# Performance work log

Hardware: AMD Instinct MI355X
Metric: run time of the kernel (lower is better)

## Reference

```python
import jax, jax.numpy as jnp
import numpy as np

B, C, H, W = 4, 64, 64, 64
NUM_HEADS = 4
INTER = 64
OUT_PLANE = 64
TOP_K = 5
BN_EPS = 1e-5


def setup_inputs() -> dict:
    key = jax.random.key(0)
    ks = jax.random.split(key, 24)
    d = {}
    d['x'] = jax.random.normal(ks[0], (B, C, H, W), dtype=jnp.float32)
    oc = INTER * NUM_HEADS
    s_in = 1.0 / np.sqrt(C)
    s_oc = 1.0 / np.sqrt(oc)
    s_op = 1.0 / np.sqrt(OUT_PLANE)
    d['wk'] = jax.random.normal(ks[1], (oc, C), dtype=jnp.float32) * s_in
    d['bk'] = jax.random.normal(ks[2], (oc,), dtype=jnp.float32) * s_in
    d['wq'] = jax.random.normal(ks[3], (oc, C), dtype=jnp.float32) * s_in
    d['bq'] = jax.random.normal(ks[4], (oc,), dtype=jnp.float32) * s_in
    d['wv'] = jax.random.normal(ks[5], (oc, C), dtype=jnp.float32) * s_in
    d['bv'] = jax.random.normal(ks[6], (oc,), dtype=jnp.float32) * s_in
    d['wp'] = jax.random.normal(ks[7], (OUT_PLANE, oc), dtype=jnp.float32) * s_oc
    d['bp'] = jax.random.normal(ks[8], (OUT_PLANE,), dtype=jnp.float32) * s_oc
    d['w1'] = jax.random.normal(ks[9], (OUT_PLANE, OUT_PLANE), dtype=jnp.float32) * s_op
    d['b1'] = jax.random.normal(ks[10], (OUT_PLANE,), dtype=jnp.float32) * s_op
    d['w2'] = jax.random.normal(ks[11], (OUT_PLANE, OUT_PLANE), dtype=jnp.float32) * s_op
    d['b2'] = jax.random.normal(ks[12], (OUT_PLANE,), dtype=jnp.float32) * s_op
    d['g1'] = 1.0 + 0.1 * jax.random.normal(ks[13], (OUT_PLANE,), dtype=jnp.float32)
    d['beta1'] = 0.1 * jax.random.normal(ks[14], (OUT_PLANE,), dtype=jnp.float32)
    d['m1'] = 0.1 * jax.random.normal(ks[15], (OUT_PLANE,), dtype=jnp.float32)
    d['v1'] = 1.0 + 0.1 * jax.random.uniform(ks[16], (OUT_PLANE,), dtype=jnp.float32)
    d['g2'] = 1.0 + 0.1 * jax.random.normal(ks[17], (OUT_PLANE,), dtype=jnp.float32)
    d['beta2'] = 0.1 * jax.random.normal(ks[18], (OUT_PLANE,), dtype=jnp.float32)
    d['m2'] = 0.1 * jax.random.normal(ks[19], (OUT_PLANE,), dtype=jnp.float32)
    d['v2'] = 1.0 + 0.1 * jax.random.uniform(ks[20], (OUT_PLANE,), dtype=jnp.float32)
    return d


def _conv1x1(x, w, b):
    return jnp.einsum('bchw,oc->bohw', x, w) + b[None, :, None, None]


def _l2norm(x, axis):
    n = jnp.sqrt(jnp.sum(x * x, axis=axis, keepdims=True))
    return x / jnp.maximum(n, 1e-12)


def _bn(x, g, be, m, v):
    scale = g / jnp.sqrt(v + BN_EPS)
    return (x - m[None, :, None, None]) * scale[None, :, None, None] + be[None, :, None, None]


def _laplacian(topk_idx, feats):
    # topk_idx: (b, N, K) int32; feats: (b, heads, N, F)
    b, heads, N, Fd = feats.shape
    K = topk_idx.shape[-1]
    src = jnp.repeat(jnp.arange(N), K)  # (N*K,)

    def one(idx, f):  # idx (N,K), f (heads,N,F)
        dst = idx.reshape(-1)  # (N*K,)
        # A = topk edges + self-loops; row degrees (dim=1 sum)
        deg = jnp.zeros((N,), feats.dtype).at[src].add(1.0) + 1.0
        norm = jnp.maximum(deg ** -0.5, 1e-9)
        w = norm[src] * norm[dst]  # (N*K,)
        gathered = f[:, dst, :] * w[None, :, None]  # (heads, N*K, F)
        agg = jax.vmap(lambda g_: jnp.zeros((N, Fd), feats.dtype).at[src].add(g_))(gathered)
        # self-loop contribution (value 1, norm[i]^2)
        return agg + (norm * norm)[None, :, None] * f

    return jax.vmap(one)(topk_idx, feats)


def reference(x, wk, bk, wq, bq, wv, bv, wp, bp, w1, b1, w2, b2,
              g1, beta1, m1, v1, g2, beta2, m2, v2):
    b, c, h, w = x.shape
    N = h * w
    # q/k/v: (b, heads, N, inter)
    k = _conv1x1(x, wk, bk).reshape(b, NUM_HEADS, INTER, N).transpose(0, 1, 3, 2)
    q = _conv1x1(x, wq, bq).reshape(b, NUM_HEADS, INTER, N).transpose(0, 1, 3, 2)
    v = _conv1x1(x, wv, bv).reshape(b, NUM_HEADS, INTER, N).transpose(0, 1, 3, 2)
    k = _l2norm(k, -1)
    q = _l2norm(q, -1)
    # hypergraph: cosine similarity over channels, top-k neighbors per node
    x_flat = x.reshape(b, c, N)
    xn = _l2norm(x_flat, 1)
    sim = jnp.einsum('bcn,bcm->bnm', xn, xn)  # (b, N, N)
    _, idx = jax.lax.top_k(sim, TOP_K)  # (b, N, K)
    k = _laplacian(idx, k)
    v = _laplacian(idx, v)
    # hydra attention: kv summed over nodes, broadcast back over q
    kv = jnp.einsum('bhnf,bhnf->bhf', k, v)[:, :, None, :]  # (b, heads, 1, inter)
    hy = q * kv  # (b, heads, N, inter)
    hy = hy.transpose(0, 1, 3, 2).reshape(b, NUM_HEADS * INTER, h, w)
    out = _conv1x1(hy, wp, bp)
    out = jax.nn.relu(_bn(_conv1x1(out, w1, b1), g1, beta1, m1, v1))
    out = jax.nn.relu(_bn(_conv1x1(out, w2, b2), g2, beta2, m2, v2))
    return out
```

## Files before the change

kernel.cpp:

```cpp
#include <hip/hip_runtime.h>
#include <math.h>

#define NB 4
#define NC 64
#define NN 4096
#define NH 4

typedef __attribute__((ext_vector_type(8))) short bf16x8;
typedef __attribute__((ext_vector_type(4))) float f32x4;

__device__ __forceinline__ unsigned int bf16rne(float v) {
    unsigned int u = __float_as_uint(v);
    return (u + 0x7fffu + ((u >> 16) & 1u)) >> 16;
}

__device__ __forceinline__ void ins5k(unsigned int (&tk)[5], unsigned int key) {
    unsigned int n0 = max(tk[0], key);
    unsigned int n1 = min(tk[0], max(tk[1], key));
    unsigned int n2 = min(tk[1], max(tk[2], key));
    unsigned int n3 = min(tk[2], max(tk[3], key));
    unsigned int n4 = min(tk[3], max(tk[4], key));
    tk[0]=n0; tk[1]=n1; tk[2]=n2; tk[3]=n3; tk[4]=n4;
}

__device__ __forceinline__ void split8(const float* v, uint4& hw4, uint4& lw4) {
    unsigned int hw[4], lw[4];
    #pragma unroll
    for (int p = 0; p < 4; ++p) {
        float v0 = v[p*2], v1 = v[p*2+1];
        unsigned int h0 = bf16rne(v0), h1 = bf16rne(v1);
        float r0 = v0 - __uint_as_float(h0 << 16);
        float r1 = v1 - __uint_as_float(h1 << 16);
        unsigned int l0 = bf16rne(r0), l1 = bf16rne(r1);
        hw[p] = h0 | (h1 << 16);
        lw[p] = l0 | (l1 << 16);
    }
    hw4 = make_uint4(hw[0], hw[1], hw[2], hw[3]);
    lw4 = make_uint4(lw[0], lw[1], lw[2], lw[3]);
}

__global__ __launch_bounds__(256) void k_pre(
    const float* __restrict__ x,
    const float* __restrict__ wk, const float* __restrict__ wq, const float* __restrict__ wv,
    unsigned short* __restrict__ hl, float* __restrict__ nrm,
    unsigned short* __restrict__ wsb)
{
    __shared__ float redn[4][64];
    int blk = blockIdx.x;
    int t = threadIdx.x;
    if (blk >= 256) {
        int r = (blk - 256)*256 + t;
        int mat = r >> 8, oc = r & 255;
        const float* wsrc = (mat==0) ? wk : ((mat==1) ? wq : wv);
        float wrow[64];
        #pragma unroll
        for (int g = 0; g < 16; ++g)
            *(float4*)&wrow[g*4] = *(const float4*)(wsrc + (size_t)oc*64 + g*4);
        unsigned short* wo = wsb + (size_t)r*128;
        #pragma unroll
        for (int g = 0; g < 8; ++g) {
            uint4 hw4, lw4;
            split8(&wrow[g*8], hw4, lw4);
            *(uint4*)(wo + g*8)      = hw4;
            *(uint4*)(wo + 64 + g*8) = lw4;
        }
        return;
    }
    int lane = t & 63, g = t >> 6;
    int node = blk*64 + lane;
    const float* xb = x + ((size_t)(node >> 12))*NC*NN + (node & (NN-1));
    float vals[16];
    float ss = 0.f;
    #pragma unroll
    for (int i = 0; i < 16; ++i) {
        vals[i] = xb[(size_t)(g*16 + i)*NN];
        ss += vals[i]*vals[i];
    }
    redn[g][lane] = ss;
    __syncthreads();
    float st = redn[0][lane] + redn[1][lane] + redn[2][lane] + redn[3][lane];
    float rn = 1.f / fmaxf(sqrtf(st), 1e-12f);
    if (g == 0) nrm[node] = sqrtf(st);
    float nv[16];
    #pragma unroll
    for (int i = 0; i < 16; ++i) nv[i] = vals[i] * rn;
    unsigned short* ho = hl + (size_t)node*128 + g*16;
    #pragma unroll
    for (int gg = 0; gg < 2; ++gg) {
        uint4 hw4, lw4;
        split8(&nv[gg*8], hw4, lw4);
        *(uint4*)(ho + gg*8)      = hw4;
        *(uint4*)(ho + 64 + gg*8) = lw4;
    }
}

__global__ __launch_bounds__(256, 2) void k_qkv(
    const unsigned short* __restrict__ hl, const float* __restrict__ nrm,
    const unsigned short* __restrict__ wsb,
    const float* __restrict__ bk, const float* __restrict__ bq, const float* __restrict__ bv,
    float* __restrict__ qo, float* __restrict__ ko, float* __restrict__ vo)
{
    int blk = blockIdx.x;
    int nt  = blk & 63;
    int rem = blk >> 6;
    int mat = rem % 3, b = rem / 3;
    const float* bias = (mat==0) ? bk : ((mat==1) ? bq : bv);
    float* outp       = (mat==0) ? ko : ((mat==1) ? qo : vo);
    int t = threadIdx.x, lane = t & 63, h = t >> 6;
    int ln = lane & 15, kh = lane >> 4;

    bf16x8 ah0[4], ah1[4], al0[4], al1[4];
    const unsigned short* wb2 = wsb + ((size_t)(mat*256 + h*64 + ln))*128 + kh*8;
    #pragma unroll
    for (int s = 0; s < 4; ++s) {
        const unsigned short* p = wb2 + (size_t)s*16*128;
        ah0[s] = *(const bf16x8*)(p);
        ah1[s] = *(const bf16x8*)(p + 32);
        al0[s] = *(const bf16x8*)(p + 64);
        al1[s] = *(const bf16x8*)(p + 96);
    }
    float4 bj[4];
    #pragma unroll
    for (int s = 0; s < 4; ++s) bj[s] = *(const float4*)(bias + h*64 + s*16 + kh*4);

    int n0base = nt*64;
    const unsigned short* xb2 = hl + ((size_t)b*NN + n0base + ln)*128 + kh*8;
    #pragma unroll
    for (int j = 0; j < 4; ++j) {
        const unsigned short* p = xb2 + (size_t)j*16*128;
        bf16x8 bh0 = *(const bf16x8*)(p);
        bf16x8 bh1 = *(const bf16x8*)(p + 32);
        bf16x8 bl0 = *(const bf16x8*)(p + 64);
        bf16x8 bl1 = *(const bf16x8*)(p + 96);
        int n = n0base + j*16 + ln;
        float sc = nrm[(size_t)b*NN + n];
        f32x4 av[4];
        #pragma unroll
        for (int s = 0; s < 4; ++s) {
            f32x4 acc = {0.f, 0.f, 0.f, 0.f};
            acc = __builtin_amdgcn_mfma_f32_16x16x32_bf16(ah0[s], bh0, acc, 0,0,0);
            acc = __builtin_amdgcn_mfma_f32_16x16x32_bf16(ah1[s], bh1, acc, 0,0,0);
            acc = __builtin_amdgcn_mfma_f32_16x16x32_bf16(al0[s], bh0, acc, 0,0,0);
            acc = __builtin_amdgcn_mfma_f32_16x16x32_bf16(al1[s], bh1, acc, 0,0,0);
            acc = __builtin_amdgcn_mfma_f32_16x16x32_bf16(ah0[s], bl0, acc, 0,0,0);
            acc = __builtin_amdgcn_mfma_f32_16x16x32_bf16(ah1[s], bl1, acc, 0,0,0);
            av[s][0] = acc[0]*sc + bj[s].x;
            av[s][1] = acc[1]*sc + bj[s].y;
            av[s][2] = acc[2]*sc + bj[s].z;
            av[s][3] = acc[3]*sc + bj[s].w;
        }
        float* ob = outp + (((size_t)(b*NH + h))*NN + n)*64 + kh*4;
        if (mat != 2) {
            float ss = 0.f;
            #pragma unroll
            for (int s = 0; s < 4; ++s)
                ss += av[s][0]*av[s][0] + av[s][1]*av[s][1]
                    + av[s][2]*av[s][2] + av[s][3]*av[s][3];
            ss += __shfl_xor(ss, 16);
            ss += __shfl_xor(ss, 32);
            float rn = 1.f / fmaxf(sqrtf(ss), 1e-12f);
            #pragma unroll
            for (int s = 0; s < 4; ++s)
                *(float4*)(ob + s*16) = make_float4(av[s][0]*rn, av[s][1]*rn,
                                                    av[s][2]*rn, av[s][3]*rn);
        } else {
            #pragma unroll
            for (int s = 0; s < 4; ++s)
                *(float4*)(ob + s*16) = make_float4(av[s][0], av[s][1],
                                                    av[s][2], av[s][3]);
        }
    }
}

__device__ __forceinline__ void ctile(const bf16x8& ah0, const bf16x8& ah1,
                                      const bf16x8& al0, const bf16x8& al1,
                                      const bf16x8& bh0, const bf16x8& bh1,
                                      const bf16x8& bl0, const bf16x8& bl1,
                                      unsigned int (&tk)[4][5], unsigned int inv)
{
    f32x4 accP = {2.0f, 2.0f, 2.0f, 2.0f};
    f32x4 accQ = {0.f, 0.f, 0.f, 0.f};
    f32x4 accR = {0.f, 0.f, 0.f, 0.f};
    accP = __builtin_amdgcn_mfma_f32_16x16x32_bf16(ah0, bh0, accP, 0,0,0);
    accQ = __builtin_amdgcn_mfma_f32_16x16x32_bf16(al0, bh0, accQ, 0,0,0);
    accR = __builtin_amdgcn_mfma_f32_16x16x32_bf16(ah0, bl0, accR, 0,0,0);
    accP = __builtin_amdgcn_mfma_f32_16x16x32_bf16(ah1, bh1, accP, 0,0,0);
    accQ = __builtin_amdgcn_mfma_f32_16x16x32_bf16(al1, bh1, accQ, 0,0,0);
    accR = __builtin_amdgcn_mfma_f32_16x16x32_bf16(ah1, bl1, accR, 0,0,0);
    #pragma unroll
    for (int r = 0; r < 4; ++r) {
        float v = (accP[r] + accQ[r]) + accR[r];
        unsigned int key = (__float_as_uint(v) & 0xFFFFF000u) | inv;
        ins5k(tk[r], key);
    }
}

__global__ __launch_bounds__(256, 2)
void k_topk(const unsigned short* __restrict__ hl, unsigned int* __restrict__ pk)
{
    int blk = blockIdx.x;
    int cs = blk & 7;
    int rg = (blk >> 3) & 15;
    int b  = blk >> 7;
    int t = threadIdx.x, lane = t & 63, wave = t >> 6;
    int ln = lane & 15, kh = lane >> 4;
    const unsigned short* hb = hl + (size_t)b*NN*128;

    const unsigned short* ap0 = hb + (size_t)(rg*256 + wave*64 + ln)*128 + kh*8;
    bf16x8 a0h0 = *(const bf16x8*)(ap0);
    bf16x8 a0h1 = *(const bf16x8*)(ap0 + 32);
    bf16x8 a0l0 = *(const bf16x8*)(ap0 + 64);
    bf16x8 a0l1 = *(const bf16x8*)(ap0 + 96);
    const unsigned short* ap1 = ap0 + 16*128;
    bf16x8 a1h0 = *(const bf16x8*)(ap1);
    bf16x8 a1h1 = *(const bf16x8*)(ap1 + 32);
    bf16x8 a1l0 = *(const bf16x8*)(ap1 + 64);
    bf16x8 a1l1 = *(const bf16x8*)(ap1 + 96);
    const unsigned short* ap2 = ap0 + 32*128;
    bf16x8 a2h0 = *(const bf16x8*)(ap2);
    bf16x8 a2h1 = *(const bf16x8*)(ap2 + 32);
    bf16x8 a2l0 = *(const bf16x8*)(ap2 + 64);
    bf16x8 a2l1 = *(const bf16x8*)(ap2 + 96);
    const unsigned short* ap3 = ap0 + 48*128;
    bf16x8 a3h0 = *(const bf16x8*)(ap3);
    bf16x8 a3h1 = *(const bf16x8*)(ap3 + 32);
    bf16x8 a3l0 = *(const bf16x8*)(ap3 + 64);
    bf16x8 a3l1 = *(const bf16x8*)(ap3 + 96);

    unsigned int tk0[4][5], tk1[4][5], tk2[4][5], tk3[4][5];
    #pragma unroll
    for (int r=0;r<4;++r)
        #pragma unroll
        for (int kk=0;kk<5;++kk) { tk0[r][kk]=0u; tk1[r][kk]=0u; tk2[r][kk]=0u; tk3[r][kk]=0u; }

    int colbase = cs*512;
    unsigned int inv0 = 4095u - (unsigned int)(colbase + ln);

    const unsigned short* bp = hb + (size_t)(colbase + ln)*128 + kh*8;
    bf16x8 Ah0 = *(const bf16x8*)(bp);
    bf16x8 Ah1 = *(const bf16x8*)(bp + 32);
    bf16x8 Al0 = *(const bf16x8*)(bp + 64);
    bf16x8 Al1 = *(const bf16x8*)(bp + 96);
    bf16x8 Bh0, Bh1, Bl0, Bl1;

    for (int t5 = 0; t5 < 32; t5 += 2) {
        {
            const unsigned short* p = bp + (size_t)(t5+1)*16*128;
            Bh0 = *(const bf16x8*)(p);
            Bh1 = *(const bf16x8*)(p + 32);
            Bl0 = *(const bf16x8*)(p + 64);
            Bl1 = *(const bf16x8*)(p + 96);
        }
        {
            unsigned int inv = inv0 - (unsigned int)(t5*16);
            ctile(a0h0,a0h1,a0l0,a0l1, Ah0,Ah1,Al0,Al1, tk0, inv);
            ctile(a1h0,a1h1,a1l0,a1l1, Ah0,Ah1,Al0,Al1, tk1, inv);
            ctile(a2h0,a2h1,a2l0,a2l1, Ah0,Ah1,Al0,Al1, tk2, inv);
            ctile(a3h0,a3h1,a3l0,a3l1, Ah0,Ah1,Al0,Al1, tk3, inv);
        }
        {
            int m = (t5+2 < 32) ? (t5+2) : 0;
            const unsigned short* p = bp + (size_t)m*16*128;
            Ah0 = *(const bf16x8*)(p);
            Ah1 = *(const bf16x8*)(p + 32);
            Al0 = *(const bf16x8*)(p + 64);
            Al1 = *(const bf16x8*)(p + 96);
        }
        {
            unsigned int inv = inv0 - (unsigned int)((t5+1)*16);
            ctile(a0h0,a0h1,a0l0,a0l1, Bh0,Bh1,Bl0,Bl1, tk0, inv);
            ctile(a1h0,a1h1,a1l0,a1l1, Bh0,Bh1,Bl0,Bl1, tk1, inv);
            ctile(a2h0,a2h1,a2l0,a2l1, Bh0,Bh1,Bl0,Bl1, tk2, inv);
            ctile(a3h0,a3h1,a3l0,a3l1, Bh0,Bh1,Bl0,Bl1, tk3, inv);
        }
    }

    #pragma unroll
    for (int m = 1; m < 16; m <<= 1) {
        #pragma unroll
        for (int r=0;r<4;++r) {
            unsigned int o0[5], o1[5], o2[5], o3[5];
            #pragma unroll
            for (int kk=0;kk<5;++kk) {
                o0[kk] = (unsigned int)__shfl_xor((int)tk0[r][kk], m);
                o1[kk] = (unsigned int)__shfl_xor((int)tk1[r][kk], m);
                o2[kk] = (unsigned int)__shfl_xor((int)tk2[r][kk], m);
                o3[kk] = (unsigned int)__shfl_xor((int)tk3[r][kk], m);
            }
            #pragma unroll
            for (int kk=0;kk<5;++kk) {
                ins5k(tk0[r], o0[kk]); ins5k(tk1[r], o1[kk]);
                ins5k(tk2[r], o2[kk]); ins5k(tk3[r], o3[kk]);
            }
        }
    }
    if (ln == 0) {
        int rowb = rg*256 + wave*64 + kh*4;
        #pragma unroll
        for (int r=0;r<4;++r) {
            size_t b0 = (((size_t)b*NN + rowb + r)*8 + cs)*5;
            size_t b1 = (((size_t)b*NN + rowb + 16 + r)*8 + cs)*5;
            size_t b2 = (((size_t)b*NN + rowb + 32 + r)*8 + cs)*5;
            size_t b3 = (((size_t)b*NN + rowb + 48 + r)*8 + cs)*5;
            #pragma unroll
            for (int kk=0;kk<5;++kk) {
                pk[b0+kk] = tk0[r][kk]; pk[b1+kk] = tk1[r][kk];
                pk[b2+kk] = tk2[r][kk]; pk[b3+kk] = tk3[r][kk];
            }
        }
    }
}

__global__ __launch_bounds__(256) void k_kv(const float* __restrict__ ko, const float* __restrict__ vo,
                                            const unsigned int* __restrict__ pk, float* __restrict__ part)
{
    int blk = blockIdx.x;
    int chunk = blk & 31, bh = blk >> 5, b = bh >> 2;
    int t = threadIdx.x;
    __shared__ int idxl[128][5];
    __shared__ float red[4][64];
    if (t < 128) {
        int n = chunk*128 + t;
        const uint4* pp = (const uint4*)(pk + ((size_t)b*NN + n)*40);
        unsigned int bk5[5] = {0u,0u,0u,0u,0u};
        #pragma unroll
        for (int e = 0; e < 10; ++e) {
            uint4 v4 = pp[e];
            ins5k(bk5, v4.x); ins5k(bk5, v4.y); ins5k(bk5, v4.z); ins5k(bk5, v4.w);
        }
        #pragma unroll
        for (int kk=0;kk<5;++kk) idxl[t][kk] = 4095 - (int)(bk5[kk] & 0xFFFu);
    }
    __syncthreads();
    int f = t & 63, g = t >> 6;
    const float* kb = ko + (size_t)bh*NN*64;
    const float* vb = vo + (size_t)bh*NN*64;
    float acc = 0.f;
    for (int i2 = 0; i2 < 32; ++i2) {
        int nl = g*32 + i2;
        int n = chunk*128 + nl;
        const int* ip = idxl[nl];
        int j0 = ip[0], j1 = ip[1], j2 = ip[2], j3 = ip[3], j4 = ip[4];
        float lk = kb[(size_t)n*64+f] + kb[(size_t)j0*64+f] + kb[(size_t)j1*64+f]
                 + kb[(size_t)j2*64+f] + kb[(size_t)j3*64+f] + kb[(size_t)j4*64+f];
        float lv = vb[(size_t)n*64+f] + vb[(size_t)j0*64+f] + vb[(size_t)j1*64+f]
                 + vb[(size_t)j2*64+f] + vb[(size_t)j3*64+f] + vb[(size_t)j4*64+f];
        acc += lk*lv;
    }
    red[g][f] = acc;
    __syncthreads();
    if (t < 64) {
        float s2 = red[0][t] + red[1][t] + red[2][t] + red[3][t];
        part[((size_t)bh*64 + t)*32 + chunk] = s2;
    }
}

__global__ __launch_bounds__(256) void k_out(
    const float* __restrict__ qo, const float* __restrict__ wp, const float* __restrict__ part,
    const float* __restrict__ bp,
    const float* __restrict__ w1, const float* __restrict__ b1,
    const float* __restrict__ w2, const float* __restrict__ b2,
    const float* __restrict__ g1, const float* __restrict__ be1,
    const float* __restrict__ m1, const float* __restrict__ v1,
    const float* __restrict__ g2, const float* __restrict__ be2,
    const float* __restrict__ m2, const float* __restrict__ v2,
    float* __restrict__ outp)
{
    int b  = blockIdx.x >> 6;
    int n0 = (blockIdx.x & 63)*64;
    __shared__ __align__(16) float qs[256*68];
    __shared__ __align__(16) float ws2[256*68];
    __shared__ __align__(16) float t0[64*68];
    int t = threadIdx.x;
    {
        int f = t & 63, sub = t >> 6;
        #pragma unroll
        for (int h = 0; h < 4; ++h) {
            const float* qb = qo + (((size_t)(b*4+h))*NN + n0)*64 + f;
            for (int nl = sub; nl < 64; nl += 4)
                qs[(h*64+f)*68 + nl] = qb[(size_t)nl*64];
        }
    }
    {
        const float* pp = part + ((size_t)b*256 + t)*32;
        float s = 0.f;
        #pragma unroll
        for (int c2 = 0; c2 < 32; ++c2) s += pp[c2];
        float kvv = s * (1.f/36.f);
        for (int o = 0; o < 64; ++o)
            ws2[t*68 + o] = wp[(size_t)o*256 + t] * kvv;
    }
    __syncthreads();
    int tr = t >> 4, tc = t & 15;
    float acc[4][4];
    #pragma unroll
    for (int i=0;i<4;++i) {
        float bb = bp[tr*4+i];
        #pragma unroll
        for (int j=0;j<4;++j) acc[i][j] = bb;
    }
    #pragma unroll 8
    for (int hf = 0; hf < 256; ++hf) {
        float4 a4 = *(const float4*)&ws2[hf*68 + tr*4];
        float4 b4 = *(const float4*)&qs[hf*68 + tc*4];
        float av[4]={a4.x,a4.y,a4.z,a4.w}, bvv[4]={b4.x,b4.y,b4.z,b4.w};
        #pragma unroll
        for (int i=0;i<4;++i)
            #pragma unroll
            for (int j=0;j<4;++j)
                acc[i][j] += av[i]*bvv[j];
    }
    #pragma unroll
    for (int i=0;i<4;++i)
        *(float4*)&t0[(tr*4+i)*68 + tc*4] = make_float4(acc[i][0],acc[i][1],acc[i][2],acc[i][3]);
    __syncthreads();
    #pragma unroll
    for (int s = 0; s < 16; ++s) {
        int e = t + 256*s;
        ws2[(e & 63)*68 + (e >> 6)] = w1[e];
    }
    __syncthreads();
    float acc2[4][4];
    #pragma unroll
    for (int i=0;i<4;++i)
        #pragma unroll
        for (int j=0;j<4;++j) acc2[i][j] = 0.f;
    #pragma unroll 8
    for (int c = 0; c < 64; ++c) {
        float4 a4 = *(const float4*)&ws2[c*68 + tr*4];
        float4 b4 = *(const float4*)&t0[c*68 + tc*4];
        float av[4]={a4.x,a4.y,a4.z,a4.w}, bvv[4]={b4.x,b4.y,b4.z,b4.w};
        #pragma unroll
        for (int i=0;i<4;++i)
            #pragma unroll
            for (int j=0;j<4;++j)
                acc2[i][j] += av[i]*bvv[j];
    }
    #pragma unroll
    for (int i=0;i<4;++i) {
        int o = tr*4+i;
        float sc = g1[o] / sqrtf(v1[o] + 1e-5f);
        float bb = b1[o], mm = m1[o], bt = be1[o];
        float4 r;
        r.x = fmaxf((acc2[i][0]+bb-mm)*sc + bt, 0.f);
        r.y = fmaxf((acc2[i][1]+bb-mm)*sc + bt, 0.f);
        r.z = fmaxf((acc2[i][2]+bb-mm)*sc + bt, 0.f);
        r.w = fmaxf((acc2[i][3]+bb-mm)*sc + bt, 0.f);
        *(float4*)&qs[o*68 + tc*4] = r;
    }
    __syncthreads();
    #pragma unroll
    for (int s = 0; s < 16; ++s) {
        int e = t + 256*s;
        ws2[(e & 63)*68 + (e >> 6)] = w2[e];
    }
    __syncthreads();
    float acc3[4][4];
    #pragma unroll
    for (int i=0;i<4;++i)
        #pragma unroll
        for (int j=0;j<4;++j) acc3[i][j] = 0.f;
    #pragma unroll 8
    for (int c = 0; c < 64; ++c) {
        float4 a4 = *(const float4*)&ws2[c*68 + tr*4];
        float4 b4 = *(const float4*)&qs[c*68 + tc*4];
        float av[4]={a4.x,a4.y,a4.z,a4.w}, bvv[4]={b4.x,b4.y,b4.z,b4.w};
        #pragma unroll
        for (int i=0;i<4;++i)
            #pragma unroll
            for (int j=0;j<4;++j)
                acc3[i][j] += av[i]*bvv[j];
    }
    #pragma unroll
    for (int i=0;i<4;++i) {
        int o = tr*4+i;
        float sc = g2[o] / sqrtf(v2[o] + 1e-5f);
        float bb = b2[o], mm = m2[o], bt = be2[o];
        float4 r;
        r.x = fmaxf((acc3[i][0]+bb-mm)*sc + bt, 0.f);
        r.y = fmaxf((acc3[i][1]+bb-mm)*sc + bt, 0.f);
        r.z = fmaxf((acc3[i][2]+bb-mm)*sc + bt, 0.f);
        r.w = fmaxf((acc3[i][3]+bb-mm)*sc + bt, 0.f);
        *(float4*)&t0[o*68 + tc*4] = r;
    }
    __syncthreads();
    float* ob = outp + ((size_t)b*64)*NN + n0;
    #pragma unroll
    for (int s = 0; s < 16; ++s) {
        int e = t + 256*s;
        int o = e >> 6, nl = e & 63;
        ob[(size_t)o*NN + nl] = t0[o*68 + nl];
    }
}

extern "C" void kernel_launch(void* const* d_in, const int* in_sizes, int n_in,
                              void* d_out, int out_size, void* d_ws, size_t ws_size,
                              hipStream_t stream)
{
    (void)in_sizes; (void)n_in; (void)out_size; (void)ws_size;
    const float* x  = (const float*)d_in[0];
    const float* wk = (const float*)d_in[1];
    const float* bk = (const float*)d_in[2];
    const float* wq = (const float*)d_in[3];
    const float* bq = (const float*)d_in[4];
    const float* wv = (const float*)d_in[5];
    const float* bv = (const float*)d_in[6];
    const float* wp = (const float*)d_in[7];
    const float* bp = (const float*)d_in[8];
    const float* w1 = (const float*)d_in[9];
    const float* b1 = (const float*)d_in[10];
    const float* w2 = (const float*)d_in[11];
    const float* b2 = (const float*)d_in[12];
    const float* g1 = (const float*)d_in[13];
    const float* be1= (const float*)d_in[14];
    const float* m1 = (const float*)d_in[15];
    const float* v1 = (const float*)d_in[16];
    const float* g2 = (const float*)d_in[17];
    const float* be2= (const float*)d_in[18];
    const float* m2 = (const float*)d_in[19];
    const float* v2 = (const float*)d_in[20];
    float* out = (float*)d_out;

    float* ws = (float*)d_ws;
    unsigned short* hlb = (unsigned short*)ws;  ws += (size_t)NB*NN*128/2;
    unsigned short* wsb = (unsigned short*)ws;  ws += (size_t)768*128/2;
    float* nrm  = ws;  ws += (size_t)NB*NN;
    float* qbuf = ws;  ws += (size_t)NB*NH*NN*64;
    float* kbuf = ws;  ws += (size_t)NB*NH*NN*64;
    float* vbuf = ws;  ws += (size_t)NB*NH*NN*64;
    float* part = ws;  ws += (size_t)16*64*32;
    unsigned int* pk = (unsigned int*)ws;  ws += (size_t)NB*NN*40;

    k_pre<<<259, 256, 0, stream>>>(x, wk, wq, wv, hlb, nrm, wsb);
    k_qkv<<<768, 256, 0, stream>>>(hlb, nrm, wsb, bk, bq, bv, qbuf, kbuf, vbuf);
    k_topk<<<512, 256, 0, stream>>>(hlb, pk);
    k_kv<<<512, 256, 0, stream>>>(kbuf, vbuf, pk, part);
    k_out<<<256, 256, 0, stream>>>(qbuf, wp, part, bp, w1,b1, w2,b2,
                                   g1,be1,m1,v1, g2,be2,m2,v2, out);
}
```

Measured before the change: 144.4 us.

## Halve k_out tile width to double blocks and shrink shared memory

The output kernel now processes 32 nodes per block instead of 64, launching 512 blocks with much smaller shared-memory buffers. It no longer builds a kv-scaled copy of the projection weights in LDS; instead it reads wp rows directly from global memory and scales them on the fly with kv kept in LDS. The top-k similarity tile also merges the third split-precision MFMA accumulator into the first, saving registers and one add. The aim is higher occupancy and less LDS setup. In exchange each block issues more global weight loads and the per-thread tiles are smaller.

```diff
diff --git a/kernel.cpp b/kernel.cpp
--- a/kernel.cpp
+++ b/kernel.cpp
@@ -180,16 +180,15 @@
 {
     f32x4 accP = {2.0f, 2.0f, 2.0f, 2.0f};
     f32x4 accQ = {0.f, 0.f, 0.f, 0.f};
-    f32x4 accR = {0.f, 0.f, 0.f, 0.f};
     accP = __builtin_amdgcn_mfma_f32_16x16x32_bf16(ah0, bh0, accP, 0,0,0);
     accQ = __builtin_amdgcn_mfma_f32_16x16x32_bf16(al0, bh0, accQ, 0,0,0);
-    accR = __builtin_amdgcn_mfma_f32_16x16x32_bf16(ah0, bl0, accR, 0,0,0);
     accP = __builtin_amdgcn_mfma_f32_16x16x32_bf16(ah1, bh1, accP, 0,0,0);
     accQ = __builtin_amdgcn_mfma_f32_16x16x32_bf16(al1, bh1, accQ, 0,0,0);
-    accR = __builtin_amdgcn_mfma_f32_16x16x32_bf16(ah1, bl1, accR, 0,0,0);
+    accP = __builtin_amdgcn_mfma_f32_16x16x32_bf16(ah0, bl0, accP, 0,0,0);
+    accP = __builtin_amdgcn_mfma_f32_16x16x32_bf16(ah1, bl1, accP, 0,0,0);
     #pragma unroll
     for (int r = 0; r < 4; ++r) {
-        float v = (accP[r] + accQ[r]) + accR[r];
+        float v = accP[r] + accQ[r];
         unsigned int key = (__float_as_uint(v) & 0xFFFFF000u) | inv;
         ins5k(tk[r], key);
     }
@@ -366,19 +365,20 @@
     const float* __restrict__ m2, const float* __restrict__ v2,
     float* __restrict__ outp)
 {
-    int b  = blockIdx.x >> 6;
-    int n0 = (blockIdx.x & 63)*64;
-    __shared__ __align__(16) float qs[256*68];
-    __shared__ __align__(16) float ws2[256*68];
-    __shared__ __align__(16) float t0[64*68];
+    int b  = blockIdx.x >> 7;
+    int n0 = (blockIdx.x & 127)*32;
+    __shared__ __align__(16) float qs[256*36];
+    __shared__ __align__(16) float ws2[64*68];
+    __shared__ __align__(16) float t0[64*36];
+    __shared__ float kvs[256];
     int t = threadIdx.x;
     {
         int f = t & 63, sub = t >> 6;
         #pragma unroll
         for (int h = 0; h < 4; ++h) {
             const float* qb = qo + (((size_t)(b*4+h))*NN + n0)*64 + f;
-            for (int nl = sub; nl < 64; nl += 4)
-                qs[(h*64+f)*68 + nl] = qb[(size_t)nl*64];
+            for (int nl = sub; nl < 32; nl += 4)
+                qs[(h*64+f)*36 + nl] = qb[(size_t)nl*64];
         }
     }
     {
@@ -386,33 +386,39 @@
         float s = 0.f;
         #pragma unroll
         for (int c2 = 0; c2 < 32; ++c2) s += pp[c2];
-        float kvv = s * (1.f/36.f);
-        for (int o = 0; o < 64; ++o)
-            ws2[t*68 + o] = wp[(size_t)o*256 + t] * kvv;
-    }
-    __syncthreads();
-    int tr = t >> 4, tc = t & 15;
-    float acc[4][4];
-    #pragma unroll
-    for (int i=0;i<4;++i) {
-        float bb = bp[tr*4+i];
+        kvs[t] = s * (1.f/36.f);
+    }
+    __syncthreads();
+    int tr = t >> 3, tc = t & 7;
+    float acc[2][4];
+    #pragma unroll
+    for (int i=0;i<2;++i) {
+        float bb = bp[tr*2+i];
         #pragma unroll
         for (int j=0;j<4;++j) acc[i][j] = bb;
     }
-    #pragma unroll 8
-    for (int hf = 0; hf < 256; ++hf) {
-        float4 a4 = *(const float4*)&ws2[hf*68 + tr*4];
-        float4 b4 = *(const float4*)&qs[hf*68 + tc*4];
-        float av[4]={a4.x,a4.y,a4.z,a4.w}, bvv[4]={b4.x,b4.y,b4.z,b4.w};
-        #pragma unroll
-        for (int i=0;i<4;++i)
-            #pragma unroll
-            for (int j=0;j<4;++j)
-                acc[i][j] += av[i]*bvv[j];
-    }
-    #pragma unroll
-    for (int i=0;i<4;++i)
-        *(float4*)&t0[(tr*4+i)*68 + tc*4] = make_float4(acc[i][0],acc[i][1],acc[i][2],acc[i][3]);
+    const float* wr0 = wp + (size_t)(tr*2+0)*256;
+    const float* wr1 = wp + (size_t)(tr*2+1)*256;
+    for (int hfb = 0; hfb < 256; hfb += 4) {
+        float4 w04 = *(const float4*)(wr0 + hfb);
+        float4 w14 = *(const float4*)(wr1 + hfb);
+        float4 kv4 = *(const float4*)&kvs[hfb];
+        float w0a[4] = {w04.x, w04.y, w04.z, w04.w};
+        float w1a[4] = {w14.x, w14.y, w14.z, w14.w};
+        float kva[4] = {kv4.x, kv4.y, kv4.z, kv4.w};
+        #pragma unroll
+        for (int u = 0; u < 4; ++u) {
+            float a0 = w0a[u]*kva[u], a1 = w1a[u]*kva[u];
+            float4 b4 = *(const float4*)&qs[(hfb+u)*36 + tc*4];
+            acc[0][0] += a0*b4.x; acc[0][1] += a0*b4.y;
+            acc[0][2] += a0*b4.z; acc[0][3] += a0*b4.w;
+            acc[1][0] += a1*b4.x; acc[1][1] += a1*b4.y;
+            acc[1][2] += a1*b4.z; acc[1][3] += a1*b4.w;
+        }
+    }
+    #pragma unroll
+    for (int i=0;i<2;++i)
+        *(float4*)&t0[(tr*2+i)*36 + tc*4] = make_float4(acc[i][0],acc[i][1],acc[i][2],acc[i][3]);
     __syncthreads();
     #pragma unroll
     for (int s = 0; s < 16; ++s) {
@@ -420,25 +426,24 @@
         ws2[(e & 63)*68 + (e >> 6)] = w1[e];
     }
     __syncthreads();
-    float acc2[4][4];
-    #pragma unroll
-    for (int i=0;i<4;++i)
+    float acc2[2][4];
+    #pragma unroll
+    for (int i=0;i<2;++i)
         #pragma unroll
         for (int j=0;j<4;++j) acc2[i][j] = 0.f;
     #pragma unroll 8
     for (int c = 0; c < 64; ++c) {
-        float4 a4 = *(const float4*)&ws2[c*68 + tr*4];
-        float4 b4 = *(const float4*)&t0[c*68 + tc*4];
-        float av[4]={a4.x,a4.y,a4.z,a4.w}, bvv[4]={b4.x,b4.y,b4.z,b4.w};
-        #pragma unroll
-        for (int i=0;i<4;++i)
-            #pragma unroll
-            for (int j=0;j<4;++j)
-                acc2[i][j] += av[i]*bvv[j];
-    }
-    #pragma unroll
-    for (int i=0;i<4;++i) {
-        int o = tr*4+i;
+        float a0 = ws2[c*68 + tr*2];
+        float a1 = ws2[c*68 + tr*2 + 1];
+        float4 b4 = *(const float4*)&t0[c*36 + tc*4];
+        acc2[0][0] += a0*b4.x; acc2[0][1] += a0*b4.y;
+        acc2[0][2] += a0*b4.z; acc2[0][3] += a0*b4.w;
+        acc2[1][0] += a1*b4.x; acc2[1][1] += a1*b4.y;
+        acc2[1][2] += a1*b4.z; acc2[1][3] += a1*b4.w;
+    }
+    #pragma unroll
+    for (int i=0;i<2;++i) {
+        int o = tr*2+i;
         float sc = g1[o] / sqrtf(v1[o] + 1e-5f);
         float bb = b1[o], mm = m1[o], bt = be1[o];
         float4 r;
@@ -446,7 +451,7 @@
         r.y = fmaxf((acc2[i][1]+bb-mm)*sc + bt, 0.f);
         r.z = fmaxf((acc2[i][2]+bb-mm)*sc + bt, 0.f);
         r.w = fmaxf((acc2[i][3]+bb-mm)*sc + bt, 0.f);
-        *(float4*)&qs[o*68 + tc*4] = r;
+        *(float4*)&qs[o*36 + tc*4] = r;
     }
     __syncthreads();
     #pragma unroll
@@ -455,25 +460,24 @@
         ws2[(e & 63)*68 + (e >> 6)] = w2[e];
     }
     __syncthreads();
-    float acc3[4][4];
-    #pragma unroll
-    for (int i=0;i<4;++i)
+    float acc3[2][4];
+    #pragma unroll
+    for (int i=0;i<2;++i)
         #pragma unroll
         for (int j=0;j<4;++j) acc3[i][j] = 0.f;
     #pragma unroll 8
     for (int c = 0; c < 64; ++c) {
-        float4 a4 = *(const float4*)&ws2[c*68 + tr*4];
-        float4 b4 = *(const float4*)&qs[c*68 + tc*4];
-        float av[4]={a4.x,a4.y,a4.z,a4.w}, bvv[4]={b4.x,b4.y,b4.z,b4.w};
-        #pragma unroll
-        for (int i=0;i<4;++i)
-            #pragma unroll
-            for (int j=0;j<4;++j)
-                acc3[i][j] += av[i]*bvv[j];
-    }
-    #pragma unroll
-    for (int i=0;i<4;++i) {
-        int o = tr*4+i;
+        float a0 = ws2[c*68 + tr*2];
+        float a1 = ws2[c*68 + tr*2 + 1];
+        float4 b4 = *(const float4*)&qs[c*36 + tc*4];
+        acc3[0][0] += a0*b4.x; acc3[0][1] += a0*b4.y;
+        acc3[0][2] += a0*b4.z; acc3[0][3] += a0*b4.w;
+        acc3[1][0] += a1*b4.x; acc3[1][1] += a1*b4.y;
+        acc3[1][2] += a1*b4.z; acc3[1][3] += a1*b4.w;
+    }
+    #pragma unroll
+    for (int i=0;i<2;++i) {
+        int o = tr*2+i;
         float sc = g2[o] / sqrtf(v2[o] + 1e-5f);
         float bb = b2[o], mm = m2[o], bt = be2[o];
         float4 r;
@@ -481,15 +485,15 @@
         r.y = fmaxf((acc3[i][1]+bb-mm)*sc + bt, 0.f);
         r.z = fmaxf((acc3[i][2]+bb-mm)*sc + bt, 0.f);
         r.w = fmaxf((acc3[i][3]+bb-mm)*sc + bt, 0.f);
-        *(float4*)&t0[o*68 + tc*4] = r;
+        *(float4*)&t0[o*36 + tc*4] = r;
     }
     __syncthreads();
     float* ob = outp + ((size_t)b*64)*NN + n0;
     #pragma unroll
-    for (int s = 0; s < 16; ++s) {
+    for (int s = 0; s < 8; ++s) {
         int e = t + 256*s;
-        int o = e >> 6, nl = e & 63;
-        ob[(size_t)o*NN + nl] = t0[o*68 + nl];
+        int o = e >> 5, nl = e & 31;
+        ob[(size_t)o*NN + nl] = t0[o*36 + nl];
     }
 }
 
@@ -535,6 +539,6 @@
     k_qkv<<<768, 256, 0, stream>>>(hlb, nrm, wsb, bk, bq, bv, qbuf, kbuf, vbuf);
     k_topk<<<512, 256, 0, stream>>>(hlb, pk);
     k_kv<<<512, 256, 0, stream>>>(kbuf, vbuf, pk, part);
-    k_out<<<256, 256, 0, stream>>>(qbuf, wp, part, bp, w1,b1, w2,b2,
+    k_out<<<512, 256, 0, stream>>>(qbuf, wp, part, bp, w1,b1, w2,b2,
                                    g1,be1,m1,v1, g2,be2,m2,v2, out);
 }
```

After: 138.6 us. 4.0% less time.
